# Kernel optimization log

Measured on AMD Instinct MI355X. Metric: run time of the kernel, lower is better.

The kernel has to match this reference:

```python
import jax, jax.numpy as jnp
import numpy as np

N = 65536          # nodes
E = N * 7          # edges (avg_degree = n_edge_type = 7)
C_IN = 128
C_OUT = 128
N_EDGE_TYPE = 7
N_NODE_TYPE = 5
FEAT = C_IN + N_NODE_TYPE  # 133, channels after one-hot concat


def setup_inputs() -> dict:
    key = jax.random.key(0)
    k1, k2, k3, k4, k5 = jax.random.split(key, 5)
    x = jax.random.normal(k1, (N, C_IN), dtype=jnp.float32)
    edge_idx = jax.random.randint(k2, (2, E), 0, N, dtype=jnp.int64)
    edge_type = jax.random.randint(k3, (E,), 0, N_EDGE_TYPE, dtype=jnp.int64)
    node_type = jax.random.randint(k4, (N,), 0, N_NODE_TYPE, dtype=jnp.int64)
    # uniform init a la module's reset_parameters
    fan_in = 7 * C_IN
    fan_out = 7 * C_OUT
    a = np.sqrt(3.0) * np.sqrt(2.0 / (fan_in + fan_out))
    weights = jax.random.uniform(k5, (N_EDGE_TYPE * FEAT, C_OUT), dtype=jnp.float32,
                                 minval=-a, maxval=a)
    return {"x": x, "edge_idx": edge_idx, "edge_type": edge_type,
            "node_type": node_type, "weights": weights}


def reference(x, edge_idx, edge_type, node_type, weights):
    # one-hot node type concat (n_node_type > 1 branch)
    one_hot = jax.nn.one_hot(node_type, N_NODE_TYPE, dtype=x.dtype)
    xa = jnp.concatenate([x, one_hot], axis=1)          # [N, FEAT]
    row, col = edge_idx[0], edge_idx[1]
    seg = row * N_EDGE_TYPE + edge_type                 # [E]
    gathered = xa[col]                                  # [E, FEAT]
    num_seg = N * N_EDGE_TYPE
    sums = jax.ops.segment_sum(gathered, seg, num_segments=num_seg)
    cnt = jax.ops.segment_sum(jnp.ones((E,), dtype=xa.dtype), seg, num_segments=num_seg)
    col_data = sums / jnp.maximum(cnt, 1.0)[:, None]    # scatter_mean
    # overwrite self-loop slot (last edge type) with node's own features
    self_idx = jnp.arange(N, dtype=jnp.int64) * N_EDGE_TYPE + (N_EDGE_TYPE - 1)
    col_data = col_data.at[self_idx].set(xa)
    out = col_data.reshape(N, N_EDGE_TYPE * FEAT) @ weights  # [N, C_OUT]
    return out
```

## Files before the change

kernel.cpp:

```cpp
#include <hip/hip_runtime.h>
#include <hip/hip_bf16.h>

#define N_NODES 65536
#define N_EDGES (N_NODES * 7)
#define NSEG    (N_NODES * 7)
#define CAP     12

typedef short short8 __attribute__((ext_vector_type(8)));
typedef float f32x4  __attribute__((ext_vector_type(4)));

__device__ __forceinline__ unsigned short f2bf(float f) {
    unsigned u = __float_as_uint(f);
    unsigned r = (u + 0x7FFFu + ((u >> 16) & 1u)) >> 16;
    return (unsigned short)r;
}
__device__ __forceinline__ unsigned pack2(float lo, float hi) {
    return (unsigned)f2bf(lo) | ((unsigned)f2bf(hi) << 16);
}
__device__ __forceinline__ float bf2f(short s) {
    return __uint_as_float(((unsigned)(unsigned short)s) << 16);
}

__global__ __launch_bounds__(256) void k_prep(const float* __restrict__ x,
                                              const int* __restrict__ ntype,
                                              const float* __restrict__ W,
                                              unsigned short* __restrict__ xb,
                                              unsigned char* __restrict__ ntb,
                                              unsigned short* __restrict__ wb,
                                              unsigned* __restrict__ cnt) {
    int i = blockIdx.x * 256 + threadIdx.x;
    {
        int row = i >> 4, mm = i & 15;
        const f32x4* p = reinterpret_cast<const f32x4*>(x + (size_t)row * 128 + mm * 8);
        f32x4 v0 = p[0], v1 = p[1];
        uint4 w;
        w.x = pack2(v0[0], v0[1]); w.y = pack2(v0[2], v0[3]);
        w.z = pack2(v1[0], v1[1]); w.w = pack2(v1[2], v1[3]);
        reinterpret_cast<uint4*>(xb)[i] = w;
    }
    if (i < N_NODES) ntb[i] = (unsigned char)ntype[i];
    if (i < 143360) {
        int j    = i & 7;
        int lane = (i >> 3) & 63;
        int cb   = (i >> 9) & 7;
        int tkc  = i >> 12;
        int kc   = tkc % 5;
        int t    = tkc / 5;
        int k = kc * 32 + ((lane >> 4) << 3) + j;
        int c = cb * 16 + (lane & 15);
        float v = (k < 133) ? W[(t * 133 + k) * 128 + c] : 0.0f;
        wb[i] = f2bf(v);
    }
    if (i < NSEG) cnt[i] = 0u;
}

__global__ __launch_bounds__(256) void k_sw(const int* __restrict__ eidx,
                                            const int* __restrict__ etype,
                                            unsigned* __restrict__ cnt,
                                            unsigned short* __restrict__ scol) {
    int e = blockIdx.x * 256 + threadIdx.x;
    int t = etype[e];
    if (t >= 6) return;
    int r = eidx[e];
    int c = eidx[N_EDGES + e];
    unsigned seg = (unsigned)r * 7u + (unsigned)t;
    unsigned slot = atomicAdd(&cnt[seg], 1u);
    if (slot < CAP) scol[seg * CAP + slot] = (unsigned short)c;
}

__global__ __launch_bounds__(512, 4) void k_main(const unsigned short* __restrict__ xb,
                                                 const unsigned char* __restrict__ ntb,
                                                 const unsigned* __restrict__ cnt,
                                                 const unsigned short* __restrict__ scol,
                                                 const unsigned short* __restrict__ wb,
                                                 float* __restrict__ out) {
    __shared__ unsigned short sA[7 * 32 * 160];

    const int tid  = threadIdx.x;
    const int lane = tid & 63;
    const int wid  = tid >> 6;
    const int n0   = blockIdx.x * 32;
    const int r    = tid >> 4;
    const int m    = tid & 15;
    const int n    = n0 + r;

    for (int i = tid; i < 7 * 32 * 12; i += 512) {
        int row = i / 12, j = i - row * 12;
        reinterpret_cast<unsigned*>(sA)[row * 80 + 68 + j] = 0u;
    }

    unsigned cv = 0;
    if (m < 7) cv = cnt[n * 7 + m];
    unsigned c_t[6];
    #pragma unroll
    for (int t = 0; t < 6; ++t) c_t[t] = (unsigned)__shfl((int)cv, (lane & 48) + t);

    uint2 q2[6];
    #pragma unroll
    for (int t = 0; t < 6; ++t)
        q2[t] = *reinterpret_cast<const uint2*>(scol + ((size_t)n * 7 + t) * CAP);

    short8 xA[6], xB[6], xS;
    #pragma unroll
    for (int t = 0; t < 6; ++t) {
        unsigned cA = (c_t[t] >= 1u) ? (q2[t].x & 0xffffu) : 0u;
        unsigned cB = (c_t[t] >= 2u) ? (q2[t].x >> 16) : 0u;
        xA[t] = *reinterpret_cast<const short8*>(xb + (size_t)cA * 128 + m * 8);
        xB[t] = *reinterpret_cast<const short8*>(xb + (size_t)cB * 128 + m * 8);
    }
    xS = *reinterpret_cast<const short8*>(xb + (size_t)n * 128 + m * 8);

    unsigned ntA[6], ntB[6], ntS = 0;
    if (m == 1) {
        #pragma unroll
        for (int t = 0; t < 6; ++t) {
            unsigned cA = (c_t[t] >= 1u) ? (q2[t].x & 0xffffu) : 0u;
            unsigned cB = (c_t[t] >= 2u) ? (q2[t].x >> 16) : 0u;
            ntA[t] = ntb[cA];
            ntB[t] = ntb[cB];
        }
        ntS = ntb[n];
    }

    #pragma unroll
    for (int t = 0; t < 6; ++t) {
        const unsigned cntv = c_t[t];
        const unsigned ce = (cntv < (unsigned)CAP) ? cntv : (unsigned)CAP;
        const size_t segbase = ((size_t)n * 7 + t) * CAP;
        uint4 w;
        if (cntv <= 1u) {
            uint4 xv = *reinterpret_cast<const uint4*>(&xA[t]);
            w.x = cntv ? xv.x : 0u; w.y = cntv ? xv.y : 0u;
            w.z = cntv ? xv.z : 0u; w.w = cntv ? xv.w : 0u;
        } else {
            float a[8];
            #pragma unroll
            for (int j = 0; j < 8; ++j) a[j] = bf2f(xA[t][j]) + bf2f(xB[t][j]);
            if (ce >= 3u) {
                unsigned c2 = q2[t].y & 0xffffu;
                short8 v = *reinterpret_cast<const short8*>(xb + (size_t)c2 * 128 + m * 8);
                #pragma unroll
                for (int j = 0; j < 8; ++j) a[j] += bf2f(v[j]);
                if (ce >= 4u) {
                    unsigned c3 = q2[t].y >> 16;
                    short8 v3 = *reinterpret_cast<const short8*>(xb + (size_t)c3 * 128 + m * 8);
                    #pragma unroll
                    for (int j = 0; j < 8; ++j) a[j] += bf2f(v3[j]);
                    for (unsigned e = 4; e < ce; ++e) {
                        unsigned c = scol[segbase + e];
                        short8 ve = *reinterpret_cast<const short8*>(xb + (size_t)c * 128 + m * 8);
                        #pragma unroll
                        for (int j = 0; j < 8; ++j) a[j] += bf2f(ve[j]);
                    }
                }
            }
            const float inv = 1.0f / (float)cntv;
            w.x = pack2(a[0] * inv, a[1] * inv); w.y = pack2(a[2] * inv, a[3] * inv);
            w.z = pack2(a[4] * inv, a[5] * inv); w.w = pack2(a[6] * inv, a[7] * inv);
        }
        *reinterpret_cast<uint4*>(sA + (t * 32 + r) * 160 + m * 8) = w;

        if (m == 1) {
            float o0 = 0.f, o1 = 0.f, o2 = 0.f, o3 = 0.f, o4 = 0.f;
            if (cntv >= 1u) { unsigned u = ntA[t];
                o0 += (u == 0); o1 += (u == 1); o2 += (u == 2); o3 += (u == 3); o4 += (u == 4); }
            if (cntv >= 2u) { unsigned u = ntB[t];
                o0 += (u == 0); o1 += (u == 1); o2 += (u == 2); o3 += (u == 3); o4 += (u == 4); }
            if (ce >= 3u) {
                unsigned u = ntb[q2[t].y & 0xffffu];
                o0 += (u == 0); o1 += (u == 1); o2 += (u == 2); o3 += (u == 3); o4 += (u == 4);
                if (ce >= 4u) {
                    unsigned u3 = ntb[q2[t].y >> 16];
                    o0 += (u3 == 0); o1 += (u3 == 1); o2 += (u3 == 2); o3 += (u3 == 3); o4 += (u3 == 4);
                    for (unsigned e = 4; e < ce; ++e) {
                        unsigned ue = ntb[(unsigned)scol[segbase + e]];
                        o0 += (ue == 0); o1 += (ue == 1); o2 += (ue == 2); o3 += (ue == 3); o4 += (ue == 4);
                    }
                }
            }
            const float inv = (cntv > 1u) ? (1.0f / (float)cntv) : 1.0f;
            uint4 wo;
            wo.x = pack2(o0 * inv, o1 * inv);
            wo.y = pack2(o2 * inv, o3 * inv);
            wo.z = pack2(o4 * inv, 0.f);
            wo.w = 0u;
            *reinterpret_cast<uint4*>(sA + (t * 32 + r) * 160 + 128) = wo;
        }
    }

    *reinterpret_cast<uint4*>(sA + (6 * 32 + r) * 160 + m * 8) =
        *reinterpret_cast<const uint4*>(&xS);
    if (m == 1) {
        uint4 wo;
        wo.x = pack2((float)(ntS == 0), (float)(ntS == 1));
        wo.y = pack2((float)(ntS == 2), (float)(ntS == 3));
        wo.z = pack2((float)(ntS == 4), 0.f);
        wo.w = 0u;
        *reinterpret_cast<uint4*>(sA + (6 * 32 + r) * 160 + 128) = wo;
    }

    short8 bv[2][5];
    #pragma unroll
    for (int kc = 0; kc < 5; ++kc)
        bv[0][kc] = *reinterpret_cast<const short8*>(
            wb + ((((0 * 5 + kc) * 8 + wid) << 6) + lane) * 8);

    __syncthreads();

    f32x4 acc0 = {0.f, 0.f, 0.f, 0.f};
    f32x4 acc1 = {0.f, 0.f, 0.f, 0.f};
    const int ar = lane & 15;
    const int hi = (lane >> 4) << 3;

    #pragma unroll
    for (int t = 0; t < 7; ++t) {
        const int cur = t & 1, nxt = cur ^ 1;
        if (t < 6) {
            #pragma unroll
            for (int kc = 0; kc < 5; ++kc)
                bv[nxt][kc] = *reinterpret_cast<const short8*>(
                    wb + (((((t + 1) * 5 + kc) * 8 + wid) << 6) + lane) * 8);
        }
        #pragma unroll
        for (int kc = 0; kc < 5; ++kc) {
            short8 a0 = *reinterpret_cast<const short8*>(
                sA + (t * 32 + ar) * 160 + kc * 32 + hi);
            short8 a1 = *reinterpret_cast<const short8*>(
                sA + (t * 32 + 16 + ar) * 160 + kc * 32 + hi);
            acc0 = __builtin_amdgcn_mfma_f32_16x16x32_bf16(a0, bv[cur][kc], acc0, 0, 0, 0);
            acc1 = __builtin_amdgcn_mfma_f32_16x16x32_bf16(a1, bv[cur][kc], acc1, 0, 0, 0);
        }
    }

    const int orow = n0 + ((lane >> 4) << 2);
    const int ocol = (wid << 4) + (lane & 15);
    #pragma unroll
    for (int rr = 0; rr < 4; ++rr) {
        out[(size_t)(orow + rr) * 128 + ocol]      = acc0[rr];
        out[(size_t)(orow + 16 + rr) * 128 + ocol] = acc1[rr];
    }
}


extern "C" void kernel_launch(void* const* d_in, const int* in_sizes, int n_in,
                              void* d_out, int out_size, void* d_ws, size_t ws_size,
                              hipStream_t stream) {
    const float* x     = (const float*)d_in[0];
    const int*   eidx  = (const int*)d_in[1];
    const int*   etype = (const int*)d_in[2];
    const int*   ntype = (const int*)d_in[3];
    const float* W     = (const float*)d_in[4];
    float* out = (float*)d_out;

    unsigned short* xb   = (unsigned short*)d_ws;
    unsigned short* wb   = (unsigned short*)((char*)d_ws + 16777216);
    unsigned char*  ntb  = (unsigned char*)((char*)d_ws + 17063936);
    unsigned*       cnt  = (unsigned*)((char*)d_ws + 17129472);
    unsigned short* scol = (unsigned short*)((char*)d_ws + 18964480);

    k_prep<<<4096,          256, 0, stream>>>(x, ntype, W, xb, ntb, wb, cnt);
    k_sw  <<<N_EDGES / 256, 256, 0, stream>>>(eidx, etype, cnt, scol);
    k_main<<<N_NODES / 32,  512, 0, stream>>>(xb, ntb, cnt, scol, wb, out);
}
```

Baseline: 92.55 us.

## Fuse edge scatter into prep kernel and pack node-type counts into 64-bit atomics

Merges the separate edge scatter kernel into the prep kernel and replaces the per-segment count zeroing with a memset. Each edge's 64-bit atomic now adds both the edge count and a per-node-type histogram field. The main kernel can then build the one-hot mean from that packed word instead of gathering node types per neighbor. It also pads the shared A-tile row stride from 160 to 168 to reduce LDS bank conflicts, and makes the small-count aggregation branchless. The cost is wider 64-bit atomics and an extra memset operation on the stream.

Result: faster. 84.25 us (-9.0%).

```diff
diff --git a/kernel.cpp b/kernel.cpp
--- a/kernel.cpp
+++ b/kernel.cpp
@@ -17,18 +17,34 @@
 __device__ __forceinline__ unsigned pack2(float lo, float hi) {
     return (unsigned)f2bf(lo) | ((unsigned)f2bf(hi) << 16);
 }
-__device__ __forceinline__ float bf2f(short s) {
-    return __uint_as_float(((unsigned)(unsigned short)s) << 16);
-}
-
-__global__ __launch_bounds__(256) void k_prep(const float* __restrict__ x,
-                                              const int* __restrict__ ntype,
-                                              const float* __restrict__ W,
-                                              unsigned short* __restrict__ xb,
-                                              unsigned char* __restrict__ ntb,
-                                              unsigned short* __restrict__ wb,
-                                              unsigned* __restrict__ cnt) {
+__device__ __forceinline__ float bflo(unsigned d) { return __uint_as_float(d << 16); }
+__device__ __forceinline__ float bfhi(unsigned d) { return __uint_as_float(d & 0xffff0000u); }
+
+__global__ __launch_bounds__(256) void k_big(const float* __restrict__ x,
+                                             const int* __restrict__ eidx,
+                                             const int* __restrict__ etype,
+                                             const int* __restrict__ ntype,
+                                             const float* __restrict__ W,
+                                             unsigned short* __restrict__ xb,
+                                             unsigned short* __restrict__ wb,
+                                             unsigned long long* __restrict__ seg64,
+                                             unsigned short* __restrict__ scol) {
     int i = blockIdx.x * 256 + threadIdx.x;
+
+    if (i < N_EDGES) {
+        int t = etype[i];
+        if (t < 6) {
+            int r = eidx[i];
+            int c = eidx[N_EDGES + i];
+            int u = ntype[c];
+            unsigned seg = (unsigned)r * 7u + (unsigned)t;
+            unsigned long long inc = 1ull | (1ull << (8 + 10 * u));
+            unsigned long long old = atomicAdd(&seg64[seg], inc);
+            unsigned slot = (unsigned)(old & 0xffull);
+            if (slot < CAP) scol[seg * CAP + slot] = (unsigned short)c;
+        }
+    }
+
     {
         int row = i >> 4, mm = i & 15;
         const f32x4* p = reinterpret_cast<const f32x4*>(x + (size_t)row * 128 + mm * 8);
@@ -38,7 +54,7 @@
         w.z = pack2(v1[0], v1[1]); w.w = pack2(v1[2], v1[3]);
         reinterpret_cast<uint4*>(xb)[i] = w;
     }
-    if (i < N_NODES) ntb[i] = (unsigned char)ntype[i];
+
     if (i < 143360) {
         int j    = i & 7;
         int lane = (i >> 3) & 63;
@@ -51,30 +67,15 @@
         float v = (k < 133) ? W[(t * 133 + k) * 128 + c] : 0.0f;
         wb[i] = f2bf(v);
     }
-    if (i < NSEG) cnt[i] = 0u;
-}
-
-__global__ __launch_bounds__(256) void k_sw(const int* __restrict__ eidx,
-                                            const int* __restrict__ etype,
-                                            unsigned* __restrict__ cnt,
-                                            unsigned short* __restrict__ scol) {
-    int e = blockIdx.x * 256 + threadIdx.x;
-    int t = etype[e];
-    if (t >= 6) return;
-    int r = eidx[e];
-    int c = eidx[N_EDGES + e];
-    unsigned seg = (unsigned)r * 7u + (unsigned)t;
-    unsigned slot = atomicAdd(&cnt[seg], 1u);
-    if (slot < CAP) scol[seg * CAP + slot] = (unsigned short)c;
 }
 
 __global__ __launch_bounds__(512, 4) void k_main(const unsigned short* __restrict__ xb,
-                                                 const unsigned char* __restrict__ ntb,
-                                                 const unsigned* __restrict__ cnt,
+                                                 const int* __restrict__ ntype,
+                                                 const unsigned long long* __restrict__ seg64,
                                                  const unsigned short* __restrict__ scol,
                                                  const unsigned short* __restrict__ wb,
                                                  float* __restrict__ out) {
-    __shared__ unsigned short sA[7 * 32 * 160];
+    __shared__ unsigned short sA[7 * 32 * 168];
 
     const int tid  = threadIdx.x;
     const int lane = tid & 63;
@@ -86,14 +87,21 @@
 
     for (int i = tid; i < 7 * 32 * 12; i += 512) {
         int row = i / 12, j = i - row * 12;
-        reinterpret_cast<unsigned*>(sA)[row * 80 + 68 + j] = 0u;
-    }
-
-    unsigned cv = 0;
-    if (m < 7) cv = cnt[n * 7 + m];
-    unsigned c_t[6];
-    #pragma unroll
-    for (int t = 0; t < 6; ++t) c_t[t] = (unsigned)__shfl((int)cv, (lane & 48) + t);
+        reinterpret_cast<unsigned*>(sA)[row * 84 + 68 + j] = 0u;
+    }
+
+    unsigned vlo = 0u, vhi = 0u;
+    if (m < 7) {
+        uint2 v = reinterpret_cast<const uint2*>(seg64)[n * 7 + m];
+        vlo = v.x; vhi = v.y;
+    }
+    unsigned clo[6], chi[6], c_t[6];
+    #pragma unroll
+    for (int t = 0; t < 6; ++t) {
+        clo[t] = (unsigned)__shfl((int)vlo, (lane & 48) + t);
+        chi[t] = (unsigned)__shfl((int)vhi, (lane & 48) + t);
+        c_t[t] = clo[t] & 0xffu;
+    }
 
     uint2 q2[6];
     #pragma unroll
@@ -103,107 +111,88 @@
     short8 xA[6], xB[6], xS;
     #pragma unroll
     for (int t = 0; t < 6; ++t) {
-        unsigned cA = (c_t[t] >= 1u) ? (q2[t].x & 0xffffu) : 0u;
-        unsigned cB = (c_t[t] >= 2u) ? (q2[t].x >> 16) : 0u;
+        unsigned cA = (c_t[t] >= 1u) ? (q2[t].x & 0xffffu) : (unsigned)n;
+        unsigned cB = (c_t[t] >= 2u) ? (q2[t].x >> 16)     : (unsigned)n;
         xA[t] = *reinterpret_cast<const short8*>(xb + (size_t)cA * 128 + m * 8);
         xB[t] = *reinterpret_cast<const short8*>(xb + (size_t)cB * 128 + m * 8);
     }
     xS = *reinterpret_cast<const short8*>(xb + (size_t)n * 128 + m * 8);
-
-    unsigned ntA[6], ntB[6], ntS = 0;
-    if (m == 1) {
-        #pragma unroll
-        for (int t = 0; t < 6; ++t) {
-            unsigned cA = (c_t[t] >= 1u) ? (q2[t].x & 0xffffu) : 0u;
-            unsigned cB = (c_t[t] >= 2u) ? (q2[t].x >> 16) : 0u;
-            ntA[t] = ntb[cA];
-            ntB[t] = ntb[cB];
-        }
-        ntS = ntb[n];
-    }
+    const int ntS = ntype[n];
 
     #pragma unroll
     for (int t = 0; t < 6; ++t) {
         const unsigned cntv = c_t[t];
-        const unsigned ce = (cntv < (unsigned)CAP) ? cntv : (unsigned)CAP;
-        const size_t segbase = ((size_t)n * 7 + t) * CAP;
-        uint4 w;
-        if (cntv <= 1u) {
-            uint4 xv = *reinterpret_cast<const uint4*>(&xA[t]);
-            w.x = cntv ? xv.x : 0u; w.y = cntv ? xv.y : 0u;
-            w.z = cntv ? xv.z : 0u; w.w = cntv ? xv.w : 0u;
-        } else {
-            float a[8];
-            #pragma unroll
-            for (int j = 0; j < 8; ++j) a[j] = bf2f(xA[t][j]) + bf2f(xB[t][j]);
-            if (ce >= 3u) {
+        const float inv = (cntv > 1u) ? __builtin_amdgcn_rcpf((float)cntv) : 1.0f;
+
+        uint4 a4 = *reinterpret_cast<const uint4*>(&xA[t]);
+        uint4 b4 = *reinterpret_cast<const uint4*>(&xB[t]);
+        a4.x = (cntv >= 1u) ? a4.x : 0u; a4.y = (cntv >= 1u) ? a4.y : 0u;
+        a4.z = (cntv >= 1u) ? a4.z : 0u; a4.w = (cntv >= 1u) ? a4.w : 0u;
+        b4.x = (cntv >= 2u) ? b4.x : 0u; b4.y = (cntv >= 2u) ? b4.y : 0u;
+        b4.z = (cntv >= 2u) ? b4.z : 0u; b4.w = (cntv >= 2u) ? b4.w : 0u;
+
+        float a[8];
+        a[0] = bflo(a4.x) + bflo(b4.x); a[1] = bfhi(a4.x) + bfhi(b4.x);
+        a[2] = bflo(a4.y) + bflo(b4.y); a[3] = bfhi(a4.y) + bfhi(b4.y);
+        a[4] = bflo(a4.z) + bflo(b4.z); a[5] = bfhi(a4.z) + bfhi(b4.z);
+        a[6] = bflo(a4.w) + bflo(b4.w); a[7] = bfhi(a4.w) + bfhi(b4.w);
+
+        if (cntv >= 3u) {
+            const unsigned ce = (cntv < (unsigned)CAP) ? cntv : (unsigned)CAP;
+            {
                 unsigned c2 = q2[t].y & 0xffffu;
                 short8 v = *reinterpret_cast<const short8*>(xb + (size_t)c2 * 128 + m * 8);
-                #pragma unroll
-                for (int j = 0; j < 8; ++j) a[j] += bf2f(v[j]);
-                if (ce >= 4u) {
-                    unsigned c3 = q2[t].y >> 16;
-                    short8 v3 = *reinterpret_cast<const short8*>(xb + (size_t)c3 * 128 + m * 8);
-                    #pragma unroll
-                    for (int j = 0; j < 8; ++j) a[j] += bf2f(v3[j]);
-                    for (unsigned e = 4; e < ce; ++e) {
-                        unsigned c = scol[segbase + e];
-                        short8 ve = *reinterpret_cast<const short8*>(xb + (size_t)c * 128 + m * 8);
-                        #pragma unroll
-                        for (int j = 0; j < 8; ++j) a[j] += bf2f(ve[j]);
-                    }
+                uint4 v4 = *reinterpret_cast<const uint4*>(&v);
+                a[0] += bflo(v4.x); a[1] += bfhi(v4.x);
+                a[2] += bflo(v4.y); a[3] += bfhi(v4.y);
+                a[4] += bflo(v4.z); a[5] += bfhi(v4.z);
+                a[6] += bflo(v4.w); a[7] += bfhi(v4.w);
+            }
+            if (ce >= 4u) {
+                unsigned c3 = q2[t].y >> 16;
+                short8 v = *reinterpret_cast<const short8*>(xb + (size_t)c3 * 128 + m * 8);
+                uint4 v4 = *reinterpret_cast<const uint4*>(&v);
+                a[0] += bflo(v4.x); a[1] += bfhi(v4.x);
+                a[2] += bflo(v4.y); a[3] += bfhi(v4.y);
+                a[4] += bflo(v4.z); a[5] += bfhi(v4.z);
+                a[6] += bflo(v4.w); a[7] += bfhi(v4.w);
+                const size_t segbase = ((size_t)n * 7 + t) * CAP;
+                for (unsigned e = 4; e < ce; ++e) {
+                    unsigned c = scol[segbase + e];
+                    short8 ve = *reinterpret_cast<const short8*>(xb + (size_t)c * 128 + m * 8);
+                    uint4 v4e = *reinterpret_cast<const uint4*>(&ve);
+                    a[0] += bflo(v4e.x); a[1] += bfhi(v4e.x);
+                    a[2] += bflo(v4e.y); a[3] += bfhi(v4e.y);
+                    a[4] += bflo(v4e.z); a[5] += bfhi(v4e.z);
+                    a[6] += bflo(v4e.w); a[7] += bfhi(v4e.w);
                 }
             }
-            const float inv = 1.0f / (float)cntv;
-            w.x = pack2(a[0] * inv, a[1] * inv); w.y = pack2(a[2] * inv, a[3] * inv);
-            w.z = pack2(a[4] * inv, a[5] * inv); w.w = pack2(a[6] * inv, a[7] * inv);
-        }
-        *reinterpret_cast<uint4*>(sA + (t * 32 + r) * 160 + m * 8) = w;
-
-        if (m == 1) {
-            float o0 = 0.f, o1 = 0.f, o2 = 0.f, o3 = 0.f, o4 = 0.f;
-            if (cntv >= 1u) { unsigned u = ntA[t];
-                o0 += (u == 0); o1 += (u == 1); o2 += (u == 2); o3 += (u == 3); o4 += (u == 4); }
-            if (cntv >= 2u) { unsigned u = ntB[t];
-                o0 += (u == 0); o1 += (u == 1); o2 += (u == 2); o3 += (u == 3); o4 += (u == 4); }
-            if (ce >= 3u) {
-                unsigned u = ntb[q2[t].y & 0xffffu];
-                o0 += (u == 0); o1 += (u == 1); o2 += (u == 2); o3 += (u == 3); o4 += (u == 4);
-                if (ce >= 4u) {
-                    unsigned u3 = ntb[q2[t].y >> 16];
-                    o0 += (u3 == 0); o1 += (u3 == 1); o2 += (u3 == 2); o3 += (u3 == 3); o4 += (u3 == 4);
-                    for (unsigned e = 4; e < ce; ++e) {
-                        unsigned ue = ntb[(unsigned)scol[segbase + e]];
-                        o0 += (ue == 0); o1 += (ue == 1); o2 += (ue == 2); o3 += (ue == 3); o4 += (ue == 4);
-                    }
-                }
-            }
-            const float inv = (cntv > 1u) ? (1.0f / (float)cntv) : 1.0f;
-            uint4 wo;
-            wo.x = pack2(o0 * inv, o1 * inv);
-            wo.y = pack2(o2 * inv, o3 * inv);
-            wo.z = pack2(o4 * inv, 0.f);
-            wo.w = 0u;
-            *reinterpret_cast<uint4*>(sA + (t * 32 + r) * 160 + 128) = wo;
-        }
-    }
-
-    *reinterpret_cast<uint4*>(sA + (6 * 32 + r) * 160 + m * 8) =
+        }
+
+        uint4 w;
+        w.x = pack2(a[0] * inv, a[1] * inv); w.y = pack2(a[2] * inv, a[3] * inv);
+        w.z = pack2(a[4] * inv, a[5] * inv); w.w = pack2(a[6] * inv, a[7] * inv);
+        *reinterpret_cast<uint4*>(sA + (t * 32 + r) * 168 + m * 8) = w;
+
+        if (m < 8) {
+            unsigned long long v64 = ((unsigned long long)chi[t] << 32) | (unsigned long long)clo[t];
+            float ohv = 0.0f;
+            if (m < 5) ohv = (float)((unsigned)((v64 >> (8 + 10 * m)) & 0x3ffull)) * inv;
+            sA[(t * 32 + r) * 168 + 128 + m] = f2bf(ohv);
+        }
+    }
+
+    *reinterpret_cast<uint4*>(sA + (6 * 32 + r) * 168 + m * 8) =
         *reinterpret_cast<const uint4*>(&xS);
-    if (m == 1) {
-        uint4 wo;
-        wo.x = pack2((float)(ntS == 0), (float)(ntS == 1));
-        wo.y = pack2((float)(ntS == 2), (float)(ntS == 3));
-        wo.z = pack2((float)(ntS == 4), 0.f);
-        wo.w = 0u;
-        *reinterpret_cast<uint4*>(sA + (6 * 32 + r) * 160 + 128) = wo;
-    }
+    if (m < 8)
+        sA[(6 * 32 + r) * 168 + 128 + m] =
+            (m == ntS) ? (unsigned short)0x3F80 : (unsigned short)0;
 
     short8 bv[2][5];
     #pragma unroll
     for (int kc = 0; kc < 5; ++kc)
         bv[0][kc] = *reinterpret_cast<const short8*>(
-            wb + ((((0 * 5 + kc) * 8 + wid) << 6) + lane) * 8);
+            wb + (((kc * 8 + wid) << 6) + lane) * 8);
 
     __syncthreads();
 
@@ -224,9 +213,9 @@
         #pragma unroll
         for (int kc = 0; kc < 5; ++kc) {
             short8 a0 = *reinterpret_cast<const short8*>(
-                sA + (t * 32 + ar) * 160 + kc * 32 + hi);
+                sA + (t * 32 + ar) * 168 + kc * 32 + hi);
             short8 a1 = *reinterpret_cast<const short8*>(
-                sA + (t * 32 + 16 + ar) * 160 + kc * 32 + hi);
+                sA + (t * 32 + 16 + ar) * 168 + kc * 32 + hi);
             acc0 = __builtin_amdgcn_mfma_f32_16x16x32_bf16(a0, bv[cur][kc], acc0, 0, 0, 0);
             acc1 = __builtin_amdgcn_mfma_f32_16x16x32_bf16(a1, bv[cur][kc], acc1, 0, 0, 0);
         }
@@ -252,13 +241,12 @@
     const float* W     = (const float*)d_in[4];
     float* out = (float*)d_out;
 
-    unsigned short* xb   = (unsigned short*)d_ws;
-    unsigned short* wb   = (unsigned short*)((char*)d_ws + 16777216);
-    unsigned char*  ntb  = (unsigned char*)((char*)d_ws + 17063936);
-    unsigned*       cnt  = (unsigned*)((char*)d_ws + 17129472);
-    unsigned short* scol = (unsigned short*)((char*)d_ws + 18964480);
-
-    k_prep<<<4096,          256, 0, stream>>>(x, ntype, W, xb, ntb, wb, cnt);
-    k_sw  <<<N_EDGES / 256, 256, 0, stream>>>(eidx, etype, cnt, scol);
-    k_main<<<N_NODES / 32,  512, 0, stream>>>(xb, ntb, cnt, scol, wb, out);
-}
+    unsigned short*     xb    = (unsigned short*)d_ws;
+    unsigned short*     wb    = (unsigned short*)((char*)d_ws + 16777216);
+    unsigned long long* seg64 = (unsigned long long*)((char*)d_ws + 17063936);
+    unsigned short*     scol  = (unsigned short*)((char*)d_ws + 20733952);
+
+    hipMemsetAsync(seg64, 0, NSEG * sizeof(unsigned long long), stream);
+    k_big <<<4096,         256, 0, stream>>>(x, eidx, etype, ntype, W, xb, wb, seg64, scol);
+    k_main<<<N_NODES / 32, 512, 0, stream>>>(xb, ntype, seg64, scol, wb, out);
+}
```
